# Kernel optimization log

Hardware: AMD Instinct MI355X
Metric: run time of the kernel (lower is better)

Reference implementation:

```python
import jax, jax.numpy as jnp
import numpy as np

N_WIRES = 8
DIM = 1 << N_WIRES  # 256
ENC_WIRES = [0, 1, 2, 2, 4, 5, 6, 7]  # faithful to source: wire 2 twice, wire 3 skipped

# Precompute composed CNOT-ring permutation: CNOT(0,1),(1,2),...,(6,7),(7,0)
_idx = np.arange(DIM)
_perm = _idx.copy()
for c, t in [(k, k + 1) for k in range(N_WIRES - 1)] + [(N_WIRES - 1, 0)]:
    cbit = (_idx >> (N_WIRES - 1 - c)) & 1
    P = np.where(cbit == 1, _idx ^ (1 << (N_WIRES - 1 - t)), _idx)
    _perm = _perm[P]
CNOT_PERM = jnp.asarray(_perm)
# Pauli-Z sign table per wire: (8, 256)
Z_SIGNS = jnp.asarray(1 - 2 * ((_idx[None, :] >> (N_WIRES - 1 - np.arange(N_WIRES)[:, None])) & 1)).astype(jnp.float32)


def _rx(state, wire, theta):
    """Apply RX(theta) on `wire`. state: (N, 256) complex64, theta: (N,) float."""
    N = state.shape[0]
    s = state.reshape(N, 1 << wire, 2, 1 << (N_WIRES - 1 - wire))
    half = theta * 0.5
    c = jnp.cos(half)[:, None, None]
    sn = jnp.sin(half)[:, None, None]
    a, b = s[:, :, 0, :], s[:, :, 1, :]
    top = c * a - 1j * sn * b
    bot = -1j * sn * a + c * b
    return jnp.stack([top, bot], axis=2).reshape(N, DIM)


def qlayer(tokens, theta):
    """Batched 8-qubit circuit: encoder RX(x_k), trainable RX(theta_w), CNOT ring, <Z_w>.
    tokens: (N, 8) float32 -> (N, 8) float32 expectation values."""
    N = tokens.shape[0]
    state = jnp.zeros((N, DIM), jnp.complex64).at[:, 0].set(1.0)
    for k, w in enumerate(ENC_WIRES):
        state = _rx(state, w, tokens[:, k])
    for w in range(N_WIRES):
        state = _rx(state, w, jnp.broadcast_to(theta[w], (N,)))
    state = state[:, CNOT_PERM]
    probs = state.real ** 2 + state.imag ** 2  # (N, 256)
    return probs @ Z_SIGNS.T  # (N, 8)


def setup_inputs() -> dict:
    key = jax.random.key(0)
    kx, kt = jax.random.split(key)
    x = jax.random.normal(kx, (16, 1024, 8), dtype=jnp.float32)
    theta = jax.random.uniform(kt, (8,), dtype=jnp.float32, minval=0.0, maxval=2.0 * np.pi)
    return {"x": x, "theta": theta}


def reference(x, theta):
    B, S, E = x.shape
    H, dk = 2, E // 2
    tok = x.reshape(B * S, E)
    # Original computes Q, K, V with the SAME shared q_layer on the SAME input,
    # so Q == K == V; compute once.
    qkv = qlayer(tok, theta).reshape(B, S, E)
    h = qkv.reshape(B, S, H, dk).transpose(0, 2, 1, 3)  # (B,H,S,dk)
    scores = jnp.einsum('bhqd,bhkd->bhqk', h, h) / np.sqrt(dk).astype(np.float32)
    w = jax.nn.softmax(scores, axis=-1)  # (eval mode: dropout inactive)
    attn = jnp.einsum('bhqk,bhkd->bhqd', w, h)
    concat = attn.transpose(0, 2, 1, 3).reshape(B, S, E)
    out = qlayer(concat.reshape(B * S, E), theta).reshape(B, S, E)
    return out
```

## Files before the change

kernel.cpp:

```cpp
#include <hip/hip_runtime.h>

#define SEQ 1024

static __device__ __forceinline__ int lds_addr(int k) {
    return (k << 3) + ((k >> 7) << 2);
}

static __device__ __forceinline__ void qrow(const float th[8], const float y[8], float o[8]) {
    float a[8];
    a[0] = y[0] + th[0];
    a[1] = y[1] + th[1];
    a[2] = y[2] + y[3] + th[2];
    a[3] = th[3];
    a[4] = y[4] + th[4];
    a[5] = y[5] + th[5];
    a[6] = y[6] + th[6];
    a[7] = y[7] + th[7];
    float c[8];
#pragma unroll
    for (int w = 0; w < 8; ++w) c[w] = __cosf(a[w]);
    o[1] = c[0] * c[1];
#pragma unroll
    for (int w = 2; w < 8; ++w) o[w] = o[w - 1] * c[w];
    float s = c[7];
#pragma unroll
    for (int w = 6; w >= 1; --w) s *= c[w];
    o[0] = s;
}

__global__ __launch_bounds__(256, 2) void mhaq_fused(const float* __restrict__ x,
                                                     const float* __restrict__ theta,
                                                     float* __restrict__ out) {
    __shared__ __align__(16) float h_lds[8 * SEQ + 7 * 4 + 4];

    const int b   = blockIdx.x >> 5;
    const int qof = (blockIdx.x & 31) << 5;
    const int t   = threadIdx.x;

    float th[8];
#pragma unroll
    for (int w = 0; w < 8; ++w) th[w] = theta[w];

    const float4* xb = (const float4*)(x + (size_t)b * SEQ * 8);
#pragma unroll
    for (int r = 0; r < 4; ++r) {
        const int k  = t + (r << 8);
        const float4 v0 = xb[2 * k];
        const float4 v1 = xb[2 * k + 1];
        const float y[8] = {v0.x, v0.y, v0.z, v0.w, v1.x, v1.y, v1.z, v1.w};
        float o[8];
        qrow(th, y, o);
        float4* p = (float4*)&h_lds[lds_addr(k)];
        p[0] = make_float4(o[0], o[1], o[2], o[3]);
        p[1] = make_float4(o[4], o[5], o[6], o[7]);
    }
    __syncthreads();

    const int lane  = t & 63;
    const int wv    = t >> 6;
    const int qiw   = lane >> 3;
    const int chunk = lane & 7;
    const int q     = qof + (wv << 3) + qiw;

    float qv[8];
    {
        const float* qp = &h_lds[lds_addr(q)];
#pragma unroll
        for (int d = 0; d < 8; ++d) qv[d] = qp[d] * 0.5f;
    }

    float l0 = 0.f, l1 = 0.f;
    float acc0[4] = {0.f, 0.f, 0.f, 0.f};
    float acc1[4] = {0.f, 0.f, 0.f, 0.f};

    int base = lds_addr(chunk << 7);
#pragma unroll 4
    for (int i = 0; i < 128; ++i) {
        const float4 k0 = *(const float4*)&h_lds[base];
        const float4 k1 = *(const float4*)&h_lds[base + 4];
        base += 8;
        const float s0 = qv[0] * k0.x + qv[1] * k0.y + qv[2] * k0.z + qv[3] * k0.w;
        const float s1 = qv[4] * k1.x + qv[5] * k1.y + qv[6] * k1.z + qv[7] * k1.w;
        const float e0 = __expf(s0);
        const float e1 = __expf(s1);
        l0 += e0;
        l1 += e1;
        acc0[0] += e0 * k0.x; acc0[1] += e0 * k0.y; acc0[2] += e0 * k0.z; acc0[3] += e0 * k0.w;
        acc1[0] += e1 * k1.x; acc1[1] += e1 * k1.y; acc1[2] += e1 * k1.z; acc1[3] += e1 * k1.w;
    }

#pragma unroll
    for (int m = 1; m < 8; m <<= 1) {
        l0 += __shfl_xor(l0, m);
        l1 += __shfl_xor(l1, m);
#pragma unroll
        for (int d = 0; d < 4; ++d) {
            acc0[d] += __shfl_xor(acc0[d], m);
            acc1[d] += __shfl_xor(acc1[d], m);
        }
    }

    if (chunk == 0) {
        const float inv0 = 1.0f / l0;
        const float inv1 = 1.0f / l1;
        float y[8];
#pragma unroll
        for (int d = 0; d < 4; ++d) {
            y[d]     = acc0[d] * inv0;
            y[4 + d] = acc1[d] * inv1;
        }
        float o[8];
        qrow(th, y, o);
        float4* op = (float4*)(out + ((size_t)(b * SEQ + q)) * 8);
        op[0] = make_float4(o[0], o[1], o[2], o[3]);
        op[1] = make_float4(o[4], o[5], o[6], o[7]);
    }
}

extern "C" void kernel_launch(void* const* d_in, const int* in_sizes, int n_in,
                              void* d_out, int out_size, void* d_ws, size_t ws_size,
                              hipStream_t stream) {
    const float* x     = (const float*)d_in[0];
    const float* theta = (const float*)d_in[1];
    float* out         = (float*)d_out;
    mhaq_fused<<<dim3(16 * 32), dim3(256), 0, stream>>>(x, theta, out);
}
```

Baseline: 67.99 us.

## Split keys across 16 lanes, double grid, use packed f32 math and exp2

Each wave now handles 4 queries, with each query's keys split across 16 lanes instead of 8 queries over 8 lanes. The grid doubles to 1024 blocks of 16 queries, and launch bounds allow 4 blocks per CU. The inner loop uses float2 vectors so the compiler can emit packed FMAs, and it folds log2(e) into the query scale so it can call exp2 directly. Global loads are batched before the qrow compute. The cost is that every block recomputes the full 1024-row qlayer into LDS, so this redundant prologue work doubles, and the cross-lane reduction grows by one shuffle step.

```diff
diff --git a/kernel.cpp b/kernel.cpp
--- a/kernel.cpp
+++ b/kernel.cpp
@@ -1,6 +1,8 @@
 #include <hip/hip_runtime.h>
 
 #define SEQ 1024
+
+typedef __attribute__((ext_vector_type(2))) float f2;
 
 static __device__ __forceinline__ int lds_addr(int k) {
     return (k << 3) + ((k >> 7) << 2);
@@ -28,13 +30,13 @@
     o[0] = s;
 }
 
-__global__ __launch_bounds__(256, 2) void mhaq_fused(const float* __restrict__ x,
+__global__ __launch_bounds__(256, 4) void mhaq_fused(const float* __restrict__ x,
                                                      const float* __restrict__ theta,
                                                      float* __restrict__ out) {
     __shared__ __align__(16) float h_lds[8 * SEQ + 7 * 4 + 4];
 
-    const int b   = blockIdx.x >> 5;
-    const int qof = (blockIdx.x & 31) << 5;
+    const int b   = blockIdx.x >> 6;
+    const int qof = (blockIdx.x & 63) << 4;
     const int t   = threadIdx.x;
 
     float th[8];
@@ -42,12 +44,18 @@
     for (int w = 0; w < 8; ++w) th[w] = theta[w];
 
     const float4* xb = (const float4*)(x + (size_t)b * SEQ * 8);
+    float4 v0[4], v1[4];
 #pragma unroll
     for (int r = 0; r < 4; ++r) {
-        const int k  = t + (r << 8);
-        const float4 v0 = xb[2 * k];
-        const float4 v1 = xb[2 * k + 1];
-        const float y[8] = {v0.x, v0.y, v0.z, v0.w, v1.x, v1.y, v1.z, v1.w};
+        const int k = t + (r << 8);
+        v0[r] = xb[2 * k];
+        v1[r] = xb[2 * k + 1];
+    }
+#pragma unroll
+    for (int r = 0; r < 4; ++r) {
+        const int k = t + (r << 8);
+        const float y[8] = {v0[r].x, v0[r].y, v0[r].z, v0[r].w,
+                            v1[r].x, v1[r].y, v1[r].z, v1[r].w};
         float o[8];
         qrow(th, y, o);
         float4* p = (float4*)&h_lds[lds_addr(k)];
@@ -58,56 +66,59 @@
 
     const int lane  = t & 63;
     const int wv    = t >> 6;
-    const int qiw   = lane >> 3;
-    const int chunk = lane & 7;
-    const int q     = qof + (wv << 3) + qiw;
+    const int qiw   = lane >> 4;
+    const int chunk = lane & 15;
+    const int q     = qof + (wv << 2) + qiw;
 
-    float qv[8];
+    const float qscale = 0.5f * 1.44269504f;
+    f2 qv01, qv23, qv45, qv67;
     {
         const float* qp = &h_lds[lds_addr(q)];
-#pragma unroll
-        for (int d = 0; d < 8; ++d) qv[d] = qp[d] * 0.5f;
+        qv01 = f2{qp[0], qp[1]} * qscale;
+        qv23 = f2{qp[2], qp[3]} * qscale;
+        qv45 = f2{qp[4], qp[5]} * qscale;
+        qv67 = f2{qp[6], qp[7]} * qscale;
     }
 
     float l0 = 0.f, l1 = 0.f;
-    float acc0[4] = {0.f, 0.f, 0.f, 0.f};
-    float acc1[4] = {0.f, 0.f, 0.f, 0.f};
+    f2 a01 = {0.f, 0.f}, a23 = {0.f, 0.f}, a45 = {0.f, 0.f}, a67 = {0.f, 0.f};
 
-    int base = lds_addr(chunk << 7);
+    int base = lds_addr(chunk << 6);
 #pragma unroll 4
-    for (int i = 0; i < 128; ++i) {
+    for (int i = 0; i < 64; ++i) {
         const float4 k0 = *(const float4*)&h_lds[base];
         const float4 k1 = *(const float4*)&h_lds[base + 4];
         base += 8;
-        const float s0 = qv[0] * k0.x + qv[1] * k0.y + qv[2] * k0.z + qv[3] * k0.w;
-        const float s1 = qv[4] * k1.x + qv[5] * k1.y + qv[6] * k1.z + qv[7] * k1.w;
-        const float e0 = __expf(s0);
-        const float e1 = __expf(s1);
+        const f2 k01 = {k0.x, k0.y}, k23 = {k0.z, k0.w};
+        const f2 k45 = {k1.x, k1.y}, k67 = {k1.z, k1.w};
+        const f2 d0 = qv01 * k01 + qv23 * k23;
+        const f2 d1 = qv45 * k45 + qv67 * k67;
+        const float e0 = __builtin_amdgcn_exp2f(d0.x + d0.y);
+        const float e1 = __builtin_amdgcn_exp2f(d1.x + d1.y);
         l0 += e0;
         l1 += e1;
-        acc0[0] += e0 * k0.x; acc0[1] += e0 * k0.y; acc0[2] += e0 * k0.z; acc0[3] += e0 * k0.w;
-        acc1[0] += e1 * k1.x; acc1[1] += e1 * k1.y; acc1[2] += e1 * k1.z; acc1[3] += e1 * k1.w;
+        const f2 e0v = {e0, e0}, e1v = {e1, e1};
+        a01 += e0v * k01;
+        a23 += e0v * k23;
+        a45 += e1v * k45;
+        a67 += e1v * k67;
     }
 
+    float red[10] = {l0, l1, a01.x, a01.y, a23.x, a23.y, a45.x, a45.y, a67.x, a67.y};
 #pragma unroll
-    for (int m = 1; m < 8; m <<= 1) {
-        l0 += __shfl_xor(l0, m);
-        l1 += __shfl_xor(l1, m);
+    for (int m = 1; m < 16; m <<= 1) {
 #pragma unroll
-        for (int d = 0; d < 4; ++d) {
-            acc0[d] += __shfl_xor(acc0[d], m);
-            acc1[d] += __shfl_xor(acc1[d], m);
-        }
+        for (int j = 0; j < 10; ++j) red[j] += __shfl_xor(red[j], m);
     }
 
     if (chunk == 0) {
-        const float inv0 = 1.0f / l0;
-        const float inv1 = 1.0f / l1;
+        const float inv0 = 1.0f / red[0];
+        const float inv1 = 1.0f / red[1];
         float y[8];
 #pragma unroll
         for (int d = 0; d < 4; ++d) {
-            y[d]     = acc0[d] * inv0;
-            y[4 + d] = acc1[d] * inv1;
+            y[d]     = red[2 + d] * inv0;
+            y[4 + d] = red[6 + d] * inv1;
         }
         float o[8];
         qrow(th, y, o);
@@ -123,5 +134,5 @@
     const float* x     = (const float*)d_in[0];
     const float* theta = (const float*)d_in[1];
     float* out         = (float*)d_out;
-    mhaq_fused<<<dim3(16 * 32), dim3(256), 0, stream>>>(x, theta, out);
+    mhaq_fused<<<dim3(16 * 64), dim3(256), 0, stream>>>(x, theta, out);
 }
```

Result: no change. 66.84 us (-1.7%).
